# Optimization experiments

Hardware: AMD Instinct MI355X
Metric: run time of the kernel (lower is better)

## Reference

```python
import jax, jax.numpy as jnp
import numpy as np

BN_EPS = 1e-5

def setup_inputs() -> dict:
    key = jax.random.key(0)
    k1, k2, k3 = jax.random.split(key, 3)
    B, D_IN, D_OUT = 16384, 2048, 1024
    stdv = np.sqrt(1.5 / (D_IN + D_OUT))
    x = jax.random.normal(k1, (B, D_IN), dtype=jnp.float32)
    weight = jax.random.uniform(k2, (D_OUT, D_IN), dtype=jnp.float32, minval=-stdv, maxval=stdv)
    bias = jax.random.normal(k3, (D_OUT,), dtype=jnp.float32) * 0.01
    gamma = jnp.ones((D_OUT,), dtype=jnp.float32)
    beta = jnp.zeros((D_OUT,), dtype=jnp.float32)
    return {"x": x, "weight": weight, "bias": bias, "gamma": gamma, "beta": beta}

def reference(x, weight, bias, gamma, beta):
    # STE-binarized weights: forward uses sign(w) (>=0 -> +1), grad flows via clamp(w,-1,1)
    w_sign = jnp.where(weight >= 0, 1.0, -1.0).astype(weight.dtype)
    w_clip = jnp.clip(weight, -1.0, 1.0)
    w_bin = jax.lax.stop_gradient(w_sign - w_clip) + w_clip
    # y = x @ w_bin.T + bias   -> [B, D_OUT]
    y = jnp.einsum('bi,oi->bo', x, w_bin) + bias[None, :]
    # BatchNorm1d (training mode: batch statistics, biased variance)
    mean = jnp.mean(y, axis=0)
    var = jnp.mean((y - mean) ** 2, axis=0)
    y_norm = (y - mean) * jax.lax.rsqrt(var + BN_EPS)
    return y_norm * gamma + beta
```

## Files before the change

kernel.cpp:

```cpp
#include <hip/hip_runtime.h>
#include <hip/hip_bf16.h>

typedef __attribute__((ext_vector_type(4))) float f32x4;
typedef __attribute__((ext_vector_type(8))) __bf16 bf16x8;
typedef __attribute__((ext_vector_type(4))) unsigned int uint4v;

constexpr int M = 16384;
constexpr int N = 1024;
constexpr int K = 2048;
constexpr int BM = 256, BN = 256;
constexpr int NK2 = K / 64;
constexpr float BN_EPS = 1e-5f;
constexpr int TM2 = M / BM;

#define GLOAD_LDS16(g, l)                                                      \
  __builtin_amdgcn_global_load_lds(                                            \
      (const __attribute__((address_space(1))) void*)(g),                      \
      (__attribute__((address_space(3))) void*)(l), 16, 0, 0)

#define SB0 __builtin_amdgcn_sched_barrier(0)
#define BARRIER __builtin_amdgcn_s_barrier()
#define VMC(n) asm volatile("s_waitcnt vmcnt(" #n ")" ::: "memory")
#define LGKM0 asm volatile("s_waitcnt lgkmcnt(0)" ::: "memory")

__device__ __forceinline__ unsigned sgnbf(float f) {
  return (f >= 0.f) ? 0x3F80u : 0xBF80u;
}
__global__ __launch_bounds__(256) void binw_kernel(
    const float* __restrict__ w, uint4v* __restrict__ wb) {
  size_t i = (size_t)blockIdx.x * 256 + threadIdx.x;
  const f32x4* win = (const f32x4*)w;
  f32x4 v0 = win[i * 2];
  f32x4 v1 = win[i * 2 + 1];
  uint4v o;
  o.x = sgnbf(v0[0]) | (sgnbf(v0[1]) << 16);
  o.y = sgnbf(v0[2]) | (sgnbf(v0[3]) << 16);
  o.z = sgnbf(v1[0]) | (sgnbf(v1[1]) << 16);
  o.w = sgnbf(v1[2]) | (sgnbf(v1[3]) << 16);
  wb[i] = o;
}

__global__ __launch_bounds__(512, 2) void gemm_bin_kernel(
    const float* __restrict__ Af, const unsigned short* __restrict__ B,
    float* __restrict__ Y, float* __restrict__ psum, float* __restrict__ psq) {
  __shared__ unsigned short Bs[2][16384];
  __shared__ float redsum[8][256];
  __shared__ float redsq[8][256];

  const int tid = threadIdx.x;
  const int wid = tid >> 6;
  const int lane = tid & 63;

  const int bid = blockIdx.x;
  const int swz = (bid & 7) * 32 + (bid >> 3);
  const int tm = swz >> 2, tn = swz & 3;
  const size_t m0 = (size_t)tm * BM, n0 = (size_t)tn * BN;

  const int frow = lane & 15;
  const int fcb = lane >> 4;
  const int bbase = frow * 32 + ((fcb ^ ((frow >> 1) & 3)) * 8);

  const float* pA = Af + (m0 + wid * 32 + frow) * (size_t)K + fcb * 8;

  const int gc = (lane & 3) ^ ((lane >> 3) & 3);
  const unsigned short* pBg =
      B + (n0 + wid * 16 + (lane >> 2)) * (size_t)K + gc * 8;

  f32x4 acc[2][16];
#pragma unroll
  for (int mi = 0; mi < 2; ++mi)
#pragma unroll
    for (int nj = 0; nj < 16; ++nj)
#pragma unroll
      for (int j = 0; j < 4; ++j) acc[mi][nj][j] = 0.f;

  f32x4 xr0, xr1, xr2, xr3, xr4, xr5, xr6, xr7;

#define AL(ktv)                                                                \
  {                                                                            \
    const float* p0_ = pA + (size_t)(ktv)*64;                                  \
    const float* p1_ = pA + 16 * (size_t)K + (size_t)(ktv)*64;                 \
    xr0 = *(const f32x4*)(p0_);                                   \
    xr1 = *(const f32x4*)(p0_ + 4);                                            \
    xr2 = *(const f32x4*)(p0_ + 32);                              \
    xr3 = *(const f32x4*)(p0_ + 36);                                           \
    xr4 = *(const f32x4*)(p1_);                                   \
    xr5 = *(const f32x4*)(p1_ + 4);                                            \
    xr6 = *(const f32x4*)(p1_ + 32);                              \
    xr7 = *(const f32x4*)(p1_ + 36);                                           \
  }

#define CVT1(dst, ra, rb)                                                      \
  {                                                                            \
    bf16x8 v_;                                                                 \
    _Pragma("unroll") for (int j_ = 0; j_ < 4; ++j_) {                         \
      v_[j_] = (__bf16)(ra)[j_];                                               \
      v_[4 + j_] = (__bf16)(rb)[j_];                                           \
    }                                                                          \
    dst = v_;                                                                  \
  }

#define BG(rd, ktv, NS)                                                        \
  GLOAD_LDS16(                                                                 \
      pBg + (size_t)((rd)&1) * 128 * K + (size_t)(ktv)*64 + ((rd) >> 1) * 32,  \
      &Bs[NS][((rd) >> 1) * 8192 + (((rd)&1) * 128 + wid * 16) * 32])

#define PHASE(S, ks, njh, aA, aB)                                              \
  {                                                                            \
    bf16x8 b_[8];                                                              \
    _Pragma("unroll") for (int j_ = 0; j_ < 8; ++j_) b_[j_] =                  \
        *(const bf16x8*)&Bs[S][(ks)*8192 + ((njh)*8 + j_) * 512 + bbase];      \
    __builtin_amdgcn_s_setprio(1);                                             \
    _Pragma("unroll") for (int j_ = 0; j_ < 8; ++j_) {                         \
      acc[0][(njh)*8 + j_] = __builtin_amdgcn_mfma_f32_16x16x32_bf16(          \
          aA, b_[j_], acc[0][(njh)*8 + j_], 0, 0, 0);                          \
      acc[1][(njh)*8 + j_] = __builtin_amdgcn_mfma_f32_16x16x32_bf16(          \
          aB, b_[j_], acc[1][(njh)*8 + j_], 0, 0, 0);                          \
    }                                                                          \
    __builtin_amdgcn_s_setprio(0);                                             \
    SB0;                                                                       \
  }

#define ITER(S, NS, ktv, STG)                                                  \
  {                                                                            \
    bf16x8 a00, a01, a10, a11;                                                 \
    CVT1(a00, xr0, xr1);                                                       \
    CVT1(a01, xr2, xr3);                                                       \
    CVT1(a10, xr4, xr5);                                                       \
    CVT1(a11, xr6, xr7);                                                       \
    SB0;                                                                       \
    if (STG) {                                                                 \
      BG(0, (ktv) + 1, NS);                                                    \
      BG(1, (ktv) + 1, NS);                                                    \
      BG(2, (ktv) + 1, NS);                                                    \
      BG(3, (ktv) + 1, NS);                                                    \
      AL((ktv) + 1);                                                           \
      SB0;                                                                     \
    }                                                                          \
    PHASE(S, 0, 0, a00, a10);                                                  \
    PHASE(S, 0, 1, a00, a10);                                                  \
    PHASE(S, 1, 0, a01, a11);                                                  \
    PHASE(S, 1, 1, a01, a11);                                                  \
    if (STG) {                                                                 \
      LGKM0;                                                                   \
      VMC(8);                                                                  \
      BARRIER;                                                                 \
    }                                                                          \
  }

  BG(0, 0, 0);
  BG(1, 0, 0);
  BG(2, 0, 0);
  BG(3, 0, 0);
  AL(0);
  SB0;
  VMC(8);
  BARRIER;

  for (int kt = 0; kt < NK2 - 2; kt += 2) {
    ITER(0, 1, kt, 1);
    ITER(1, 0, kt + 1, 1);
  }
  ITER(0, 1, NK2 - 2, 1);
  ITER(1, 0, NK2 - 1, 0);

#pragma unroll
  for (int nj = 0; nj < 16; ++nj) {
    float s = 0.f, q = 0.f;
#pragma unroll
    for (int mi = 0; mi < 2; ++mi)
#pragma unroll
      for (int j = 0; j < 4; ++j) {
        float v = acc[mi][nj][j];
        s += v;
        q += v * v;
      }
    s += __shfl_xor(s, 16);
    s += __shfl_xor(s, 32);
    q += __shfl_xor(q, 16);
    q += __shfl_xor(q, 32);
    if (fcb == 0) {
      redsum[wid][nj * 16 + frow] = s;
      redsq[wid][nj * 16 + frow] = q;
    }
  }
  __syncthreads();
  if (tid < BN) {
    float s = 0.f, q = 0.f;
#pragma unroll
    for (int w = 0; w < 8; ++w) {
      s += redsum[w][tid];
      q += redsq[w][tid];
    }
    psum[(size_t)tm * N + n0 + tid] = s;
    psq[(size_t)tm * N + n0 + tid] = q;
  }

#pragma unroll
  for (int mi = 0; mi < 2; ++mi) {
    const size_t r0 = m0 + wid * 32 + mi * 16 + fcb * 4;
#pragma unroll
    for (int nj = 0; nj < 16; ++nj) {
      float* yp = Y + r0 * N + n0 + nj * 16 + frow;
#pragma unroll
      for (int j = 0; j < 4; ++j) yp[(size_t)j * N] = acc[mi][nj][j];
    }
  }
}

__global__ __launch_bounds__(256) void bnstats_kernel(
    const float* __restrict__ psum, const float* __restrict__ psq,
    const float* __restrict__ gamma, const float* __restrict__ beta,
    float* __restrict__ scale, float* __restrict__ shift) {
  const int c = blockIdx.x * 256 + threadIdx.x;
  float s = 0.f, q = 0.f;
  for (int i = 0; i < TM2; ++i) {
    s += psum[i * N + c];
    q += psq[i * N + c];
  }
  const float mean = s * (1.f / (float)M);
  const float var = q * (1.f / (float)M) - mean * mean;
  const float inv = rsqrtf(var + BN_EPS);
  const float sc = gamma[c] * inv;
  scale[c] = sc;
  shift[c] = beta[c] - mean * sc;
}

__global__ __launch_bounds__(256) void bnapply_kernel(
    float* __restrict__ Y, const float* __restrict__ scale,
    const float* __restrict__ shift) {
  const size_t i = (size_t)blockIdx.x * 256 + threadIdx.x;
  f32x4 y = ((const f32x4*)Y)[i];
  const int c = (int)((i * 4) & (N - 1));
  f32x4 sc = *(const f32x4*)&scale[c];
  f32x4 sh = *(const f32x4*)&shift[c];
  ((f32x4*)Y)[i] = y * sc + sh;
}

extern "C" void kernel_launch(void* const* d_in, const int* in_sizes, int n_in,
                              void* d_out, int out_size, void* d_ws,
                              size_t ws_size, hipStream_t stream) {
  const float* x = (const float*)d_in[0];
  const float* w = (const float*)d_in[1];
  const float* gamma = (const float*)d_in[3];
  const float* beta = (const float*)d_in[4];
  float* Y = (float*)d_out;

  char* ws = (char*)d_ws;
  uint4v* wb = (uint4v*)ws;
  float* psum = (float*)(ws + (size_t)N * K * 2);
  float* psq = psum + (size_t)TM2 * N;
  float* scale = psq + (size_t)TM2 * N;
  float* shift = scale + N;

  binw_kernel<<<(N * K / 8) / 256, 256, 0, stream>>>(w, wb);
  gemm_bin_kernel<<<(M / BM) * (N / BN), 512, 0, stream>>>(
      x, (const unsigned short*)wb, Y, psum, psq);
  bnstats_kernel<<<N / 256, 256, 0, stream>>>(psum, psq, gamma, beta, scale,
                                              shift);
  bnapply_kernel<<<(M * N / 4) / 256, 256, 0, stream>>>(Y, scale, shift);
}
```

Before: 131.9 us.

## Retile GEMM to 64-row full-width blocks with LDS-staged bf16 A tiles

```diff
diff --git a/kernel.cpp b/kernel.cpp
--- a/kernel.cpp
+++ b/kernel.cpp
@@ -3,15 +3,16 @@
 
 typedef __attribute__((ext_vector_type(4))) float f32x4;
 typedef __attribute__((ext_vector_type(8))) __bf16 bf16x8;
+typedef __attribute__((ext_vector_type(4))) __bf16 bf16x4;
 typedef __attribute__((ext_vector_type(4))) unsigned int uint4v;
 
 constexpr int M = 16384;
 constexpr int N = 1024;
 constexpr int K = 2048;
-constexpr int BM = 256, BN = 256;
-constexpr int NK2 = K / 64;
+constexpr int BMR = 64;
+constexpr int NT = K / 32;
 constexpr float BN_EPS = 1e-5f;
-constexpr int TM2 = M / BM;
+constexpr int TMB = M / BMR;
 
 #define GLOAD_LDS16(g, l)                                                      \
   __builtin_amdgcn_global_load_lds(                                            \
@@ -43,132 +44,120 @@
 __global__ __launch_bounds__(512, 2) void gemm_bin_kernel(
     const float* __restrict__ Af, const unsigned short* __restrict__ B,
     float* __restrict__ Y, float* __restrict__ psum, float* __restrict__ psq) {
-  __shared__ unsigned short Bs[2][16384];
-  __shared__ float redsum[8][256];
-  __shared__ float redsq[8][256];
+  __shared__ unsigned short Bs[2][32768];
+  __shared__ unsigned short Asd[2][2048];
 
   const int tid = threadIdx.x;
   const int wid = tid >> 6;
   const int lane = tid & 63;
-
-  const int bid = blockIdx.x;
-  const int swz = (bid & 7) * 32 + (bid >> 3);
-  const int tm = swz >> 2, tn = swz & 3;
-  const size_t m0 = (size_t)tm * BM, n0 = (size_t)tn * BN;
-
   const int frow = lane & 15;
   const int fcb = lane >> 4;
-  const int bbase = frow * 32 + ((fcb ^ ((frow >> 1) & 3)) * 8);
-
-  const float* pA = Af + (m0 + wid * 32 + frow) * (size_t)K + fcb * 8;
-
-  const int gc = (lane & 3) ^ ((lane >> 3) & 3);
+  const int swq = (frow >> 1) & 3;
+
+  const int tm = blockIdx.x;
+  const size_t m0 = (size_t)tm * BMR;
+
+  const int aoff = frow * 32 + (fcb ^ swq) * 8;
+  const int boff = (wid * 128 + frow) * 32 + (fcb ^ swq) * 8;
+
+  const int bgc = (lane & 3) ^ ((lane >> 3) & 3);
   const unsigned short* pBg =
-      B + (n0 + wid * 16 + (lane >> 2)) * (size_t)K + gc * 8;
-
-  f32x4 acc[2][16];
-#pragma unroll
-  for (int mi = 0; mi < 2; ++mi)
-#pragma unroll
-    for (int nj = 0; nj < 16; ++nj)
+      B + (size_t)(wid * 128 + (lane >> 2)) * K + bgc * 8;
+
+  const int rA = tid >> 3, qA = tid & 7;
+  const float* pAg = Af + (m0 + rA) * (size_t)K + qA * 4;
+  const int awoff = rA * 32 + (((qA >> 1) ^ ((rA >> 1) & 3)) * 8) + (qA & 1) * 4;
+
+  f32x4 acc[4][8];
+#pragma unroll
+  for (int mi = 0; mi < 4; ++mi)
+#pragma unroll
+    for (int nj = 0; nj < 8; ++nj)
 #pragma unroll
       for (int j = 0; j < 4; ++j) acc[mi][nj][j] = 0.f;
 
-  f32x4 xr0, xr1, xr2, xr3, xr4, xr5, xr6, xr7;
-
-#define AL(ktv)                                                                \
+#define MFMA16(NJ0)                                                            \
+  LGKM0;                                                                       \
+  SB0;                                                                         \
+  __builtin_amdgcn_s_setprio(1);                                               \
+  _Pragma("unroll") for (int mi_ = 0; mi_ < 4; ++mi_)                          \
+      _Pragma("unroll") for (int nj_ = 0; nj_ < 4; ++nj_)                      \
+          acc[mi_][(NJ0) + nj_] = __builtin_amdgcn_mfma_f32_16x16x32_bf16(     \
+              a_[mi_], b_[nj_], acc[mi_][(NJ0) + nj_], 0, 0, 0);               \
+  __builtin_amdgcn_s_setprio(0);
+
+#define ITER(S, NS, t, MODE, XL, XC)                                           \
   {                                                                            \
-    const float* p0_ = pA + (size_t)(ktv)*64;                                  \
-    const float* p1_ = pA + 16 * (size_t)K + (size_t)(ktv)*64;                 \
-    xr0 = *(const f32x4*)(p0_);                                   \
-    xr1 = *(const f32x4*)(p0_ + 4);                                            \
-    xr2 = *(const f32x4*)(p0_ + 32);                              \
-    xr3 = *(const f32x4*)(p0_ + 36);                                           \
-    xr4 = *(const f32x4*)(p1_);                                   \
-    xr5 = *(const f32x4*)(p1_ + 4);                                            \
-    xr6 = *(const f32x4*)(p1_ + 32);                              \
-    xr7 = *(const f32x4*)(p1_ + 36);                                           \
-  }
-
-#define CVT1(dst, ra, rb)                                                      \
-  {                                                                            \
-    bf16x8 v_;                                                                 \
-    _Pragma("unroll") for (int j_ = 0; j_ < 4; ++j_) {                         \
-      v_[j_] = (__bf16)(ra)[j_];                                               \
-      v_[4 + j_] = (__bf16)(rb)[j_];                                           \
-    }                                                                          \
-    dst = v_;                                                                  \
-  }
-
-#define BG(rd, ktv, NS)                                                        \
-  GLOAD_LDS16(                                                                 \
-      pBg + (size_t)((rd)&1) * 128 * K + (size_t)(ktv)*64 + ((rd) >> 1) * 32,  \
-      &Bs[NS][((rd) >> 1) * 8192 + (((rd)&1) * 128 + wid * 16) * 32])
-
-#define PHASE(S, ks, njh, aA, aB)                                              \
-  {                                                                            \
-    bf16x8 b_[8];                                                              \
-    _Pragma("unroll") for (int j_ = 0; j_ < 8; ++j_) b_[j_] =                  \
-        *(const bf16x8*)&Bs[S][(ks)*8192 + ((njh)*8 + j_) * 512 + bbase];      \
-    __builtin_amdgcn_s_setprio(1);                                             \
-    _Pragma("unroll") for (int j_ = 0; j_ < 8; ++j_) {                         \
-      acc[0][(njh)*8 + j_] = __builtin_amdgcn_mfma_f32_16x16x32_bf16(          \
-          aA, b_[j_], acc[0][(njh)*8 + j_], 0, 0, 0);                          \
-      acc[1][(njh)*8 + j_] = __builtin_amdgcn_mfma_f32_16x16x32_bf16(          \
-          aB, b_[j_], acc[1][(njh)*8 + j_], 0, 0, 0);                          \
-    }                                                                          \
-    __builtin_amdgcn_s_setprio(0);                                             \
+    bf16x8 a_[4], b_[4];                                                       \
+    _Pragma("unroll") for (int i_ = 0; i_ < 4; ++i_) {                         \
+      a_[i_] = *(const bf16x8*)&Asd[S][aoff + i_ * 512];                       \
+      b_[i_] = *(const bf16x8*)&Bs[S][boff + i_ * 512];                        \
+    }                                                                          \
     SB0;                                                                       \
-  }
-
-#define ITER(S, NS, ktv, STG)                                                  \
-  {                                                                            \
-    bf16x8 a00, a01, a10, a11;                                                 \
-    CVT1(a00, xr0, xr1);                                                       \
-    CVT1(a01, xr2, xr3);                                                       \
-    CVT1(a10, xr4, xr5);                                                       \
-    CVT1(a11, xr6, xr7);                                                       \
+    if (MODE == 0 || MODE == 1) {                                              \
+      _Pragma("unroll") for (int u_ = 0; u_ < 8; ++u_)                         \
+          GLOAD_LDS16(pBg + (size_t)u_ * 16 * K + (size_t)((t) + 1) * 32,      \
+                      &Bs[NS][(wid * 128 + u_ * 16) * 32]);                    \
+      SB0;                                                                     \
+    }                                                                          \
+    if (MODE == 0) {                                                           \
+      XL = __builtin_nontemporal_load(                                         \
+          (const f32x4*)(pAg + (size_t)((t) + 2) * 32));                       \
+      SB0;                                                                     \
+    }                                                                          \
+    BARRIER;                                                                   \
+    MFMA16(0);                                                                 \
+    BARRIER;                                                                   \
+    _Pragma("unroll") for (int i_ = 0; i_ < 4; ++i_) b_[i_] =                  \
+        *(const bf16x8*)&Bs[S][boff + (4 + i_) * 512];                         \
     SB0;                                                                       \
-    if (STG) {                                                                 \
-      BG(0, (ktv) + 1, NS);                                                    \
-      BG(1, (ktv) + 1, NS);                                                    \
-      BG(2, (ktv) + 1, NS);                                                    \
-      BG(3, (ktv) + 1, NS);                                                    \
-      AL((ktv) + 1);                                                           \
+    if (MODE != 2) {        \
+      bf16x4 v_;                                                               \
+      _Pragma("unroll") for (int j_ = 0; j_ < 4; ++j_)                         \
+          v_[j_] = (__bf16)(XC)[j_];                                           \
+      *(bf16x4*)&Asd[NS][awoff] = v_;                                          \
       SB0;                                                                     \
     }                                                                          \
-    PHASE(S, 0, 0, a00, a10);                                                  \
-    PHASE(S, 0, 1, a00, a10);                                                  \
-    PHASE(S, 1, 0, a01, a11);                                                  \
-    PHASE(S, 1, 1, a01, a11);                                                  \
-    if (STG) {                                                                 \
-      LGKM0;                                                                   \
-      VMC(8);                                                                  \
-      BARRIER;                                                                 \
-    }                                                                          \
-  }
-
-  BG(0, 0, 0);
-  BG(1, 0, 0);
-  BG(2, 0, 0);
-  BG(3, 0, 0);
-  AL(0);
+    BARRIER;                                                                   \
+    MFMA16(4);                                                                 \
+    if (MODE == 0) VMC(1);          \
+    if (MODE == 1) VMC(0);                                                     \
+    if (MODE != 2) BARRIER;                                                    \
+  }
+
+  f32x4 xa, xb;
+  xa = __builtin_nontemporal_load((const f32x4*)pAg);
   SB0;
-  VMC(8);
+#pragma unroll
+  for (int u_ = 0; u_ < 8; ++u_)
+    GLOAD_LDS16(pBg + (size_t)u_ * 16 * K, &Bs[0][(wid * 128 + u_ * 16) * 32]);
+  SB0;
+  xb = __builtin_nontemporal_load((const f32x4*)(pAg + 32));
+  SB0;
+  {
+    bf16x4 v_;
+#pragma unroll
+    for (int j_ = 0; j_ < 4; ++j_) v_[j_] = (__bf16)xa[j_];
+    *(bf16x4*)&Asd[0][awoff] = v_;
+  }
+  VMC(1);
+  LGKM0;
   BARRIER;
 
-  for (int kt = 0; kt < NK2 - 2; kt += 2) {
-    ITER(0, 1, kt, 1);
-    ITER(1, 0, kt + 1, 1);
-  }
-  ITER(0, 1, NK2 - 2, 1);
-  ITER(1, 0, NK2 - 1, 0);
-
-#pragma unroll
-  for (int nj = 0; nj < 16; ++nj) {
+  for (int t = 0; t < NT - 4; t += 2) {
+    ITER(0, 1, t, 0, xa, xb);
+    ITER(1, 0, t + 1, 0, xb, xa);
+  }
+  ITER(0, 1, NT - 4, 0, xa, xb);
+  ITER(1, 0, NT - 3, 0, xb, xa);
+  ITER(0, 1, NT - 2, 1, xa, xb);
+  ITER(1, 0, NT - 1, 2, xa, xa);
+
+#pragma unroll
+  for (int nj = 0; nj < 8; ++nj) {
     float s = 0.f, q = 0.f;
 #pragma unroll
-    for (int mi = 0; mi < 2; ++mi)
+    for (int mi = 0; mi < 4; ++mi)
 #pragma unroll
       for (int j = 0; j < 4; ++j) {
         float v = acc[mi][nj][j];
@@ -180,30 +169,20 @@
     q += __shfl_xor(q, 16);
     q += __shfl_xor(q, 32);
     if (fcb == 0) {
-      redsum[wid][nj * 16 + frow] = s;
-      redsq[wid][nj * 16 + frow] = q;
+      psum[(size_t)tm * N + wid * 128 + nj * 16 + frow] = s;
+      psq[(size_t)tm * N + wid * 128 + nj * 16 + frow] = q;
     }
   }
-  __syncthreads();
-  if (tid < BN) {
-    float s = 0.f, q = 0.f;
-#pragma unroll
-    for (int w = 0; w < 8; ++w) {
-      s += redsum[w][tid];
-      q += redsq[w][tid];
-    }
-    psum[(size_t)tm * N + n0 + tid] = s;
-    psq[(size_t)tm * N + n0 + tid] = q;
-  }
-
-#pragma unroll
-  for (int mi = 0; mi < 2; ++mi) {
-    const size_t r0 = m0 + wid * 32 + mi * 16 + fcb * 4;
-#pragma unroll
-    for (int nj = 0; nj < 16; ++nj) {
-      float* yp = Y + r0 * N + n0 + nj * 16 + frow;
-#pragma unroll
-      for (int j = 0; j < 4; ++j) yp[(size_t)j * N] = acc[mi][nj][j];
+
+#pragma unroll
+  for (int mi = 0; mi < 4; ++mi) {
+#pragma unroll
+    for (int nj = 0; nj < 8; ++nj) {
+      float* yp =
+          Y + (m0 + mi * 16 + fcb * 4) * N + wid * 128 + nj * 16 + frow;
+#pragma unroll
+      for (int j = 0; j < 4; ++j)
+        __builtin_nontemporal_store(acc[mi][nj][j], yp + (size_t)j * N);
     }
   }
 }
@@ -213,11 +192,14 @@
     const float* __restrict__ gamma, const float* __restrict__ beta,
     float* __restrict__ scale, float* __restrict__ shift) {
   const int c = blockIdx.x * 256 + threadIdx.x;
-  float s = 0.f, q = 0.f;
-  for (int i = 0; i < TM2; ++i) {
-    s += psum[i * N + c];
-    q += psq[i * N + c];
-  }
+  float s0 = 0.f, s1 = 0.f, q0 = 0.f, q1 = 0.f;
+  for (int i = 0; i < TMB; i += 2) {
+    s0 += psum[i * N + c];
+    s1 += psum[(i + 1) * N + c];
+    q0 += psq[i * N + c];
+    q1 += psq[(i + 1) * N + c];
+  }
+  const float s = s0 + s1, q = q0 + q1;
   const float mean = s * (1.f / (float)M);
   const float var = q * (1.f / (float)M) - mean * mean;
   const float inv = rsqrtf(var + BN_EPS);
@@ -249,13 +231,13 @@
   char* ws = (char*)d_ws;
   uint4v* wb = (uint4v*)ws;
   float* psum = (float*)(ws + (size_t)N * K * 2);
-  float* psq = psum + (size_t)TM2 * N;
-  float* scale = psq + (size_t)TM2 * N;
+  float* psq = psum + (size_t)TMB * N;
+  float* scale = psq + (size_t)TMB * N;
   float* shift = scale + N;
 
   binw_kernel<<<(N * K / 8) / 256, 256, 0, stream>>>(w, wb);
-  gemm_bin_kernel<<<(M / BM) * (N / BN), 512, 0, stream>>>(
-      x, (const unsigned short*)wb, Y, psum, psq);
+  gemm_bin_kernel<<<TMB, 512, 0, stream>>>(x, (const unsigned short*)wb, Y,
+                                           psum, psq);
   bnstats_kernel<<<N / 256, 256, 0, stream>>>(psum, psq, gamma, beta, scale,
                                               shift);
   bnapply_kernel<<<(M * N / 4) / 256, 256, 0, stream>>>(Y, scale, shift);
```

Measured after the change: 183.6 us. 1.39x slower.

## Restructure GEMM to 4x2 warp grid with 32-wide K steps

Applied to the files above, without the earlier changes.

```diff
diff --git a/kernel.cpp b/kernel.cpp
--- a/kernel.cpp
+++ b/kernel.cpp
@@ -9,7 +9,7 @@
 constexpr int N = 1024;
 constexpr int K = 2048;
 constexpr int BM = 256, BN = 256;
-constexpr int NK2 = K / 64;
+constexpr int NT = K / 32;
 constexpr float BN_EPS = 1e-5f;
 constexpr int TM2 = M / BM;
 
@@ -43,13 +43,14 @@
 __global__ __launch_bounds__(512, 2) void gemm_bin_kernel(
     const float* __restrict__ Af, const unsigned short* __restrict__ B,
     float* __restrict__ Y, float* __restrict__ psum, float* __restrict__ psq) {
-  __shared__ unsigned short Bs[2][16384];
-  __shared__ float redsum[8][256];
-  __shared__ float redsq[8][256];
+  __shared__ unsigned short Bs[2][8192];
+  __shared__ float redsum[4][256];
+  __shared__ float redsq[4][256];
 
   const int tid = threadIdx.x;
   const int wid = tid >> 6;
   const int lane = tid & 63;
+  const int wr = wid >> 1, wc = wid & 1;
 
   const int bid = blockIdx.x;
   const int swz = (bid & 7) * 32 + (bid >> 3);
@@ -58,38 +59,39 @@
 
   const int frow = lane & 15;
   const int fcb = lane >> 4;
-  const int bbase = frow * 32 + ((fcb ^ ((frow >> 1) & 3)) * 8);
-
-  const float* pA = Af + (m0 + wid * 32 + frow) * (size_t)K + fcb * 8;
-
-  const int gc = (lane & 3) ^ ((lane >> 3) & 3);
+  const int swq = (frow >> 1) & 3;
+
+  const int boff = (wc * 128 + frow) * 32 + (fcb ^ swq) * 8;
+
+  const int bgc = (lane & 3) ^ ((lane >> 3) & 3);
   const unsigned short* pBg =
-      B + (n0 + wid * 16 + (lane >> 2)) * (size_t)K + gc * 8;
-
-  f32x4 acc[2][16];
-#pragma unroll
-  for (int mi = 0; mi < 2; ++mi)
-#pragma unroll
-    for (int nj = 0; nj < 16; ++nj)
+      B + (n0 + wid * 32 + (lane >> 2)) * (size_t)K + bgc * 8;
+
+  const float* pA = Af + (m0 + wr * 64 + frow) * (size_t)K + fcb * 8;
+
+  f32x4 acc[4][8];
+#pragma unroll
+  for (int mi = 0; mi < 4; ++mi)
+#pragma unroll
+    for (int nj = 0; nj < 8; ++nj)
 #pragma unroll
       for (int j = 0; j < 4; ++j) acc[mi][nj][j] = 0.f;
 
   f32x4 xr0, xr1, xr2, xr3, xr4, xr5, xr6, xr7;
-
-#define AL(ktv)                                                                \
-  {                                                                            \
-    const float* p0_ = pA + (size_t)(ktv)*64;                                  \
-    const float* p1_ = pA + 16 * (size_t)K + (size_t)(ktv)*64;                 \
-    xr0 = *(const f32x4*)(p0_);                                   \
-    xr1 = *(const f32x4*)(p0_ + 4);                                            \
-    xr2 = *(const f32x4*)(p0_ + 32);                              \
-    xr3 = *(const f32x4*)(p0_ + 36);                                           \
-    xr4 = *(const f32x4*)(p1_);                                   \
-    xr5 = *(const f32x4*)(p1_ + 4);                                            \
-    xr6 = *(const f32x4*)(p1_ + 32);                              \
-    xr7 = *(const f32x4*)(p1_ + 36);                                           \
-  }
-
+  bf16x8 af0, af1, af2, af3;
+
+#define AL(t)                                                                  \
+  {                                                                            \
+    const float* p_ = pA + (size_t)(t)*32;                                     \
+    xr0 = *(const f32x4*)(p_);                                                 \
+    xr1 = *(const f32x4*)(p_ + 4);                                             \
+    xr2 = *(const f32x4*)(p_ + 16 * (size_t)K);                                \
+    xr3 = *(const f32x4*)(p_ + 16 * (size_t)K + 4);                            \
+    xr4 = *(const f32x4*)(p_ + 32 * (size_t)K);                                \
+    xr5 = *(const f32x4*)(p_ + 32 * (size_t)K + 4);                            \
+    xr6 = *(const f32x4*)(p_ + 48 * (size_t)K);                                \
+    xr7 = *(const f32x4*)(p_ + 48 * (size_t)K + 4);                            \
+  }
 #define CVT1(dst, ra, rb)                                                      \
   {                                                                            \
     bf16x8 v_;                                                                 \
@@ -99,76 +101,72 @@
     }                                                                          \
     dst = v_;                                                                  \
   }
-
-#define BG(rd, ktv, NS)                                                        \
-  GLOAD_LDS16(                                                                 \
-      pBg + (size_t)((rd)&1) * 128 * K + (size_t)(ktv)*64 + ((rd) >> 1) * 32,  \
-      &Bs[NS][((rd) >> 1) * 8192 + (((rd)&1) * 128 + wid * 16) * 32])
-
-#define PHASE(S, ks, njh, aA, aB)                                              \
-  {                                                                            \
+#define ACVT                                                                   \
+  CVT1(af0, xr0, xr1);                                                         \
+  CVT1(af1, xr2, xr3);                                                         \
+  CVT1(af2, xr4, xr5);                                                         \
+  CVT1(af3, xr6, xr7);
+#define BG2(t, NS)                                                             \
+  {                                                                            \
+    GLOAD_LDS16(pBg + (size_t)(t)*32, &Bs[NS][(wid * 32) * 32]);               \
+    GLOAD_LDS16(pBg + 16 * (size_t)K + (size_t)(t)*32,                         \
+                &Bs[NS][(wid * 32 + 16) * 32]);                                \
+  }
+
+#define ITER(S, NS, t, MODE)                                                   \
+  {                                                                            \
+    if (MODE == 0) {                                                           \
+      AL((t) + 1);                                                             \
+      SB0;                                                                     \
+      BG2((t) + 1, NS);                                                        \
+      SB0;                                                                     \
+    }                                                                          \
     bf16x8 b_[8];                                                              \
     _Pragma("unroll") for (int j_ = 0; j_ < 8; ++j_) b_[j_] =                  \
-        *(const bf16x8*)&Bs[S][(ks)*8192 + ((njh)*8 + j_) * 512 + bbase];      \
+        *(const bf16x8*)&Bs[S][boff + j_ * 512];                               \
+    LGKM0;                                                                     \
+    SB0;                                                                       \
     __builtin_amdgcn_s_setprio(1);                                             \
-    _Pragma("unroll") for (int j_ = 0; j_ < 8; ++j_) {                         \
-      acc[0][(njh)*8 + j_] = __builtin_amdgcn_mfma_f32_16x16x32_bf16(          \
-          aA, b_[j_], acc[0][(njh)*8 + j_], 0, 0, 0);                          \
-      acc[1][(njh)*8 + j_] = __builtin_amdgcn_mfma_f32_16x16x32_bf16(          \
-          aB, b_[j_], acc[1][(njh)*8 + j_], 0, 0, 0);                          \
+    _Pragma("unroll") for (int nj_ = 0; nj_ < 8; ++nj_) {                      \
+      acc[0][nj_] = __builtin_amdgcn_mfma_f32_16x16x32_bf16(                   \
+          af0, b_[nj_], acc[0][nj_], 0, 0, 0);                                 \
+      acc[1][nj_] = __builtin_amdgcn_mfma_f32_16x16x32_bf16(                   \
+          af1, b_[nj_], acc[1][nj_], 0, 0, 0);                                 \
+      acc[2][nj_] = __builtin_amdgcn_mfma_f32_16x16x32_bf16(                   \
+          af2, b_[nj_], acc[2][nj_], 0, 0, 0);                                 \
+      acc[3][nj_] = __builtin_amdgcn_mfma_f32_16x16x32_bf16(                   \
+          af3, b_[nj_], acc[3][nj_], 0, 0, 0);                                 \
     }                                                                          \
     __builtin_amdgcn_s_setprio(0);                                             \
     SB0;                                                                       \
-  }
-
-#define ITER(S, NS, ktv, STG)                                                  \
-  {                                                                            \
-    bf16x8 a00, a01, a10, a11;                                                 \
-    CVT1(a00, xr0, xr1);                                                       \
-    CVT1(a01, xr2, xr3);                                                       \
-    CVT1(a10, xr4, xr5);                                                       \
-    CVT1(a11, xr6, xr7);                                                       \
-    SB0;                                                                       \
-    if (STG) {                                                                 \
-      BG(0, (ktv) + 1, NS);                                                    \
-      BG(1, (ktv) + 1, NS);                                                    \
-      BG(2, (ktv) + 1, NS);                                                    \
-      BG(3, (ktv) + 1, NS);                                                    \
-      AL((ktv) + 1);                                                           \
+    if (MODE == 0) {                                                           \
+      ACVT;                                                                    \
       SB0;                                                                     \
-    }                                                                          \
-    PHASE(S, 0, 0, a00, a10);                                                  \
-    PHASE(S, 0, 1, a00, a10);                                                  \
-    PHASE(S, 1, 0, a01, a11);                                                  \
-    PHASE(S, 1, 1, a01, a11);                                                  \
-    if (STG) {                                                                 \
-      LGKM0;                                                                   \
-      VMC(8);                                                                  \
+      VMC(0);                                                                  \
       BARRIER;                                                                 \
     }                                                                          \
   }
 
-  BG(0, 0, 0);
-  BG(1, 0, 0);
-  BG(2, 0, 0);
-  BG(3, 0, 0);
   AL(0);
   SB0;
-  VMC(8);
+  BG2(0, 0);
+  SB0;
+  ACVT;
+  VMC(0);
   BARRIER;
 
-  for (int kt = 0; kt < NK2 - 2; kt += 2) {
-    ITER(0, 1, kt, 1);
-    ITER(1, 0, kt + 1, 1);
-  }
-  ITER(0, 1, NK2 - 2, 1);
-  ITER(1, 0, NK2 - 1, 0);
-
-#pragma unroll
-  for (int nj = 0; nj < 16; ++nj) {
+  for (int t = 0; t < NT - 2; t += 2) {
+    ITER(0, 1, t, 0);
+    ITER(1, 0, t + 1, 0);
+  }
+  ITER(0, 1, NT - 2, 0);
+  ITER(1, 0, NT - 1, 2);
+
+#pragma unroll
+  for (int nj = 0; nj < 8; ++nj) {
     float s = 0.f, q = 0.f;
 #pragma unroll
-    for (int mi = 0; mi < 2; ++mi)
+    for (int mi = 0; mi < 4; ++mi)
 #pragma unroll
       for (int j = 0; j < 4; ++j) {
         float v = acc[mi][nj][j];
@@ -180,28 +178,24 @@
     q += __shfl_xor(q, 16);
     q += __shfl_xor(q, 32);
     if (fcb == 0) {
-      redsum[wid][nj * 16 + frow] = s;
-      redsq[wid][nj * 16 + frow] = q;
+      redsum[wr][wc * 128 + nj * 16 + frow] = s;
+      redsq[wr][wc * 128 + nj * 16 + frow] = q;
     }
   }
   __syncthreads();
   if (tid < BN) {
-    float s = 0.f, q = 0.f;
-#pragma unroll
-    for (int w = 0; w < 8; ++w) {
-      s += redsum[w][tid];
-      q += redsq[w][tid];
-    }
-    psum[(size_t)tm * N + n0 + tid] = s;
-    psq[(size_t)tm * N + n0 + tid] = q;
-  }
-
-#pragma unroll
-  for (int mi = 0; mi < 2; ++mi) {
-    const size_t r0 = m0 + wid * 32 + mi * 16 + fcb * 4;
-#pragma unroll
-    for (int nj = 0; nj < 16; ++nj) {
-      float* yp = Y + r0 * N + n0 + nj * 16 + frow;
+    psum[(size_t)tm * N + n0 + tid] =
+        redsum[0][tid] + redsum[1][tid] + redsum[2][tid] + redsum[3][tid];
+    psq[(size_t)tm * N + n0 + tid] =
+        redsq[0][tid] + redsq[1][tid] + redsq[2][tid] + redsq[3][tid];
+  }
+
+#pragma unroll
+  for (int mi = 0; mi < 4; ++mi) {
+    const size_t r0 = m0 + wr * 64 + mi * 16 + fcb * 4;
+#pragma unroll
+    for (int nj = 0; nj < 8; ++nj) {
+      float* yp = Y + r0 * N + n0 + wc * 128 + nj * 16 + frow;
 #pragma unroll
       for (int j = 0; j < 4; ++j) yp[(size_t)j * N] = acc[mi][nj][j];
     }
```

Measured after the change: 208.8 us. 1.58x slower.
